# Kernel optimization log

Hardware: AMD Instinct MI355X
Metric: run time of the kernel (lower is better)

## Reference

```python
import jax, jax.numpy as jnp
import numpy as np

CP_LEN = 256
FFT_SIZE = 1024
OFFSET = CP_LEN // 2                      # 128
PILOT_SPACING = 100
NSYMS = 824
TOTAL_SYMS = NSYMS + 1 + NSYMS // PILOT_SPACING   # 833
PAD_L = (FFT_SIZE - TOTAL_SYMS) // 2      # 95
PAD_R = FFT_SIZE - PAD_L - TOTAL_SYMS     # 96
PILOTS_IDX = np.arange(PAD_L, FFT_SIZE - PAD_R, PILOT_SPACING)  # 9 pilots

def _data_indices():
    # Statically unroll the original while-loop: gather all non-pilot data bins.
    idxs = []
    idx = 0
    jj = PAD_L + 1
    while idx < NSYMS:
        n = min(PILOT_SPACING - 1, NSYMS - idx)
        idxs.extend(range(jj, jj + n))
        idx += n
        jj += n + 1
    return np.asarray(idxs, dtype=np.int32)

DATA_IDX = _data_indices()  # [824]


def setup_inputs() -> dict:
    key = jax.random.key(0)
    # [batch, n_symbols, 2*(FFT_SIZE+CP_LEN)] interleaved I/Q floats
    in1 = jax.random.normal(key, (16, 1024, 2 * (FFT_SIZE + CP_LEN)), dtype=jnp.float32)
    return {"in1": in1}


def reference(in1):
    t = jnp.arange(FFT_SIZE, dtype=jnp.float32)
    # Deinterleave I/Q -> complex64
    iq = jax.lax.complex(in1[:, :, ::2], in1[:, :, 1::2])
    # FFT of the window starting at half the CP, then fftshift via roll
    spec = jnp.fft.fft(iq[:, :, OFFSET:OFFSET + FFT_SIZE], axis=2)
    result = jnp.roll(spec, FFT_SIZE // 2, axis=2)
    # Compensate timing-offset phase ramp
    result = result * jnp.exp(1j * OFFSET * t * (2.0 * np.pi / FFT_SIZE))
    # Estimate residual slope from pilot phase differences (wrapped to [-pi,pi])
    a = jnp.diff(jnp.angle(result[:, :, PILOTS_IDX]), axis=2)
    a = jnp.where(a > np.pi, a - 2.0 * np.pi, a)
    a = jnp.where(a < -np.pi, a + 2.0 * np.pi, a)
    mn = jnp.mean(a, axis=2)  # [B, S]
    result = result * jnp.exp(-1j * t * mn[:, :, None] / PILOT_SPACING)
    # Gather data (non-pilot) bins and interleave real/imag -> [B, S, 2*NSYMS]
    data = result[:, :, DATA_IDX]
    x = jnp.stack([data.real, data.imag], axis=-1).reshape(
        data.shape[0], data.shape[1], 2 * NSYMS)
    return x.astype(jnp.float32)
```

## Files before the change

### kernel.cpp

```cpp
#include <hip/hip_runtime.h>
#include <math.h>

#define NT      256
#define NSYMS   824
#define NPILOT  9

#define PADIDX(k) ((k) + ((k) >> 4))

#define C32_TWOPI_1024  6.1359233222901821136474609375e-3f

__device__ __forceinline__ float2 cmulf(float2 a, float2 b) {
    return make_float2(a.x * b.x - a.y * b.y, a.x * b.y + a.y * b.x);
}

template <int LM, int F>
__device__ __forceinline__ void dif_stage(float2* __restrict__ buf,
                                          const float2* __restrict__ W256,
                                          int i) {
    const int r = i & (LM - 1);
    const int base = ((i & ~(LM - 1)) << 2) | r;
    float2 a = buf[PADIDX(base)];
    float2 b = buf[PADIDX(base + LM)];
    float2 c = buf[PADIDX(base + 2 * LM)];
    float2 d = buf[PADIDX(base + 3 * LM)];
    float2 t0 = make_float2(a.x + c.x, a.y + c.y);
    float2 t1 = make_float2(a.x - c.x, a.y - c.y);
    float2 t2 = make_float2(b.x + d.x, b.y + d.y);
    float2 t3 = make_float2(b.x - d.x, b.y - d.y);
    float2 y0 = make_float2(t0.x + t2.x, t0.y + t2.y);
    float2 y1 = make_float2(t1.x + t3.y, t1.y - t3.x);
    float2 y2 = make_float2(t0.x - t2.x, t0.y - t2.y);
    float2 y3 = make_float2(t1.x - t3.y, t1.y + t3.x);
    const int e1 = F * r;
    const int e2 = 2 * F * r;
    const int e3 = 3 * F * r;
    float2 w1 = W256[PADIDX(e1)];
    float2 w2 = W256[PADIDX(e2 & 255)];
    if (e2 & 256) w2 = make_float2(w2.y, -w2.x);
    float2 w3 = W256[PADIDX(e3 & 255)];
    {
        const int q = e3 >> 8;
        if (q == 1)      w3 = make_float2(w3.y, -w3.x);
        else if (q == 2) w3 = make_float2(-w3.x, -w3.y);
    }
    buf[PADIDX(base)]          = y0;
    buf[PADIDX(base + LM)]     = cmulf(w1, y1);
    buf[PADIDX(base + 2 * LM)] = cmulf(w2, y2);
    buf[PADIDX(base + 3 * LM)] = cmulf(w3, y3);
}

__global__ void table_init(double2* __restrict__ Tg, float2* __restrict__ Wg) {
    const int t = threadIdx.x;
    double sn, cs;
    sincos((double)t * -6.1359231515425649189e-3, &sn, &cs);
    Tg[t] = make_double2(cs, sn);
    Wg[t] = make_float2((float)cs, (float)sn);
}

__global__ __launch_bounds__(NT, 8) void ofdm_kernel(const float* __restrict__ in,
                                                     float* __restrict__ out,
                                                     const double2* __restrict__ Tg,
                                                     const float2* __restrict__ Wg) {
    __shared__ double2 T256[256];
    __shared__ double2 u_s[NT];
    __shared__ float2  buf[1088];
    __shared__ float2  W256[272];
    __shared__ double2 pr2[NPILOT];
    __shared__ double  mn_s;

    const int row = blockIdx.x;
    const int tid = threadIdx.x;

    const float2* rin2 = (const float2*)(in + (size_t)row * 2560) + 128;
    float2 v0 = rin2[tid];
    float2 v1 = rin2[tid + 256];
    float2 v2 = rin2[tid + 512];
    float2 v3 = rin2[tid + 768];

    T256[tid] = Tg[tid];
    W256[PADIDX(tid)] = Wg[tid];

    double ux = ((double)v0.x - (double)v2.x) - ((double)v1.y - (double)v3.y);
    double uy = ((double)v0.y - (double)v2.y) + ((double)v1.x - (double)v3.x);

    buf[PADIDX(tid)]       = v0;
    buf[PADIDX(tid + 256)] = v1;
    buf[PADIDX(tid + 512)] = v2;
    buf[PADIDX(tid + 768)] = v3;
    u_s[tid] = make_double2(ux, uy);
    __syncthreads();

    if (tid < 16 * NPILOT) {
        const int p  = tid >> 4;
        const int g  = tid & 15;
        const int jj = 95 + 100 * p;
        const int K  = (jj + 512) & 1023;
        const double sc = (p & 1) ? -0.70710678118654752440
                                  :  0.70710678118654752440;
        int idx = (K * g) & 1023;
        const int step = (K * 16) & 1023;
        double2 acc = make_double2(0.0, 0.0);
        #pragma unroll
        for (int m = 0; m < 8; m++) {
            const int s = g + 16 * m;
            double2 u0 = u_s[s];
            double2 u1 = u_s[s + 128];
            double upx = u0.x + sc * (u1.x - u1.y);
            double upy = u0.y + sc * (u1.x + u1.y);
            double2 w  = T256[idx & 255];
            const int q = idx >> 8;
            double wx = w.x, wy = w.y;
            if (q & 1) { double t = wx; wx = wy; wy = -t; }
            if (q & 2) { wx = -wx; wy = -wy; }
            acc.x += wx * upx - wy * upy;
            acc.y += wx * upy + wy * upx;
            idx = (idx + step) & 1023;
        }
        #pragma unroll
        for (int off = 1; off < 16; off <<= 1) {
            acc.x += __shfl_xor(acc.x, off, 64);
            acc.y += __shfl_xor(acc.y, off, 64);
        }
        if (g == 0) pr2[p] = acc;
    }
    dif_stage<256, 1>(buf, W256, tid);
    __syncthreads();

    dif_stage<64, 4>(buf, W256, tid);
    if (tid >= 192) {
        const int p  = tid - 192;
        const int pc = (p < 8) ? p : 8;
        double2 acc = pr2[pc];
        const int jj = 95 + 100 * pc;
        float th32 = (float)(128 * jj) * C32_TWOPI_1024;
        double sn, cs;
        sincos((double)th32, &sn, &cs);
        double csf = (double)(float)cs;
        double snf = (double)(float)sn;
        double re = acc.x * csf - acc.y * snf;
        double im = acc.x * snf + acc.y * csf;
        double a  = atan2(im, re);
        double an = __shfl_down(a, 1, 64);
        double d  = an - a;
        if (d > 3.14159265358979323846)       d -= 6.28318530717958647693;
        else if (d < -3.14159265358979323846) d += 6.28318530717958647693;
        if (p >= 8) d = 0.0;
        d += __shfl_xor(d, 1, 64);
        d += __shfl_xor(d, 2, 64);
        d += __shfl_xor(d, 4, 64);
        if (p == 0) mn_s = d * 0.125;
    }
    __syncthreads();

    dif_stage<16, 16>(buf, W256, tid);
    __syncthreads();
    dif_stage<4, 64>(buf, W256, tid);
    __syncthreads();

    {
        const double mn001 = mn_s * 0.01;
        const int pb = PADIDX(4 * tid);
        float2 a = buf[pb];
        float2 b = buf[pb + 1];
        float2 c = buf[pb + 2];
        float2 d = buf[pb + 3];
        float2 t0 = make_float2(a.x + c.x, a.y + c.y);
        float2 t1 = make_float2(a.x - c.x, a.y - c.y);
        float2 t2 = make_float2(b.x + d.x, b.y + d.y);
        float2 t3 = make_float2(b.x - d.x, b.y - d.y);
        float2 y0 = make_float2(t0.x + t2.x, t0.y + t2.y);
        float2 y1 = make_float2(t1.x + t3.y, t1.y - t3.x);
        float2 y2 = make_float2(t0.x - t2.x, t0.y - t2.y);
        float2 y3 = make_float2(t1.x - t3.y, t1.y + t3.x);

        const int R = ((tid & 3) << 6) | (((tid >> 2) & 3) << 4) |
                      (((tid >> 4) & 3) << 2) | ((tid >> 6) & 3);

        float2* rout = (float2*)(out + (size_t)row * (2 * NSYMS));
        float2 ys[4] = { y2, y3, y0, y1 };
        #pragma unroll
        for (int k = 0; k < 4; k++) {
            const int jj = R + 256 * k;
            if (jj >= 96 && jj <= 927 && ((jj - 95) % 100) != 0) {
                const int dd = jj - 96 - (jj - 96) / 100;
                float2 z = ys[k];
                float th32 = (float)(128 * jj) * C32_TWOPI_1024;
                float ph = th32 - (float)(mn001 * (double)jj);
                float sn, cs;
                __sincosf(ph, &sn, &cs);
                rout[dd] = make_float2(z.x * cs - z.y * sn,
                                       z.x * sn + z.y * cs);
            }
        }
    }
}

extern "C" void kernel_launch(void* const* d_in, const int* in_sizes, int n_in,
                              void* d_out, int out_size, void* d_ws, size_t ws_size,
                              hipStream_t stream) {
    const float* in = (const float*)d_in[0];
    float* out = (float*)d_out;
    double2* Tg = (double2*)d_ws;
    float2*  Wg = (float2*)((char*)d_ws + 4096);
    table_init<<<dim3(1), dim3(256), 0, stream>>>(Tg, Wg);
    ofdm_kernel<<<dim3(16 * 1024), dim3(NT), 0, stream>>>(in, out, Tg, Wg);
}
```

Before: 267.5 us.

## Do first FFT stage in registers and read twiddles from global memory

```diff
diff --git a/kernel.cpp b/kernel.cpp
--- a/kernel.cpp
+++ b/kernel.cpp
@@ -15,7 +15,7 @@
 
 template <int LM, int F>
 __device__ __forceinline__ void dif_stage(float2* __restrict__ buf,
-                                          const float2* __restrict__ W256,
+                                          const float2* __restrict__ Wg,
                                           int i) {
     const int r = i & (LM - 1);
     const int base = ((i & ~(LM - 1)) << 2) | r;
@@ -34,10 +34,10 @@
     const int e1 = F * r;
     const int e2 = 2 * F * r;
     const int e3 = 3 * F * r;
-    float2 w1 = W256[PADIDX(e1)];
-    float2 w2 = W256[PADIDX(e2 & 255)];
+    float2 w1 = Wg[e1];
+    float2 w2 = Wg[e2 & 255];
     if (e2 & 256) w2 = make_float2(w2.y, -w2.x);
-    float2 w3 = W256[PADIDX(e3 & 255)];
+    float2 w3 = Wg[e3 & 255];
     {
         const int q = e3 >> 8;
         if (q == 1)      w3 = make_float2(w3.y, -w3.x);
@@ -61,10 +61,8 @@
                                                      float* __restrict__ out,
                                                      const double2* __restrict__ Tg,
                                                      const float2* __restrict__ Wg) {
-    __shared__ double2 T256[256];
     __shared__ double2 u_s[NT];
     __shared__ float2  buf[1088];
-    __shared__ float2  W256[272];
     __shared__ double2 pr2[NPILOT];
     __shared__ double  mn_s;
 
@@ -77,16 +75,33 @@
     float2 v2 = rin2[tid + 512];
     float2 v3 = rin2[tid + 768];
 
-    T256[tid] = Tg[tid];
-    W256[PADIDX(tid)] = Wg[tid];
-
     double ux = ((double)v0.x - (double)v2.x) - ((double)v1.y - (double)v3.y);
     double uy = ((double)v0.y - (double)v2.y) + ((double)v1.x - (double)v3.x);
 
-    buf[PADIDX(tid)]       = v0;
-    buf[PADIDX(tid + 256)] = v1;
-    buf[PADIDX(tid + 512)] = v2;
-    buf[PADIDX(tid + 768)] = v3;
+    {
+        const int e2 = 2 * tid, e3 = 3 * tid;
+        float2 w1 = Wg[tid];
+        float2 w2 = Wg[e2 & 255];
+        if (e2 & 256) w2 = make_float2(w2.y, -w2.x);
+        float2 w3 = Wg[e3 & 255];
+        {
+            const int q = e3 >> 8;
+            if (q == 1)      w3 = make_float2(w3.y, -w3.x);
+            else if (q == 2) w3 = make_float2(-w3.x, -w3.y);
+        }
+        float2 t0 = make_float2(v0.x + v2.x, v0.y + v2.y);
+        float2 t1 = make_float2(v0.x - v2.x, v0.y - v2.y);
+        float2 t2 = make_float2(v1.x + v3.x, v1.y + v3.y);
+        float2 t3 = make_float2(v1.x - v3.x, v1.y - v3.y);
+        float2 y0 = make_float2(t0.x + t2.x, t0.y + t2.y);
+        float2 y1 = make_float2(t1.x + t3.y, t1.y - t3.x);
+        float2 y2 = make_float2(t0.x - t2.x, t0.y - t2.y);
+        float2 y3 = make_float2(t1.x - t3.y, t1.y + t3.x);
+        buf[PADIDX(tid)]       = y0;
+        buf[PADIDX(tid + 256)] = cmulf(w1, y1);
+        buf[PADIDX(tid + 512)] = cmulf(w2, y2);
+        buf[PADIDX(tid + 768)] = cmulf(w3, y3);
+    }
     u_s[tid] = make_double2(ux, uy);
     __syncthreads();
 
@@ -107,7 +122,7 @@
             double2 u1 = u_s[s + 128];
             double upx = u0.x + sc * (u1.x - u1.y);
             double upy = u0.y + sc * (u1.x + u1.y);
-            double2 w  = T256[idx & 255];
+            double2 w  = Tg[idx & 255];
             const int q = idx >> 8;
             double wx = w.x, wy = w.y;
             if (q & 1) { double t = wx; wx = wy; wy = -t; }
@@ -123,10 +138,10 @@
         }
         if (g == 0) pr2[p] = acc;
     }
-    dif_stage<256, 1>(buf, W256, tid);
-    __syncthreads();
-
-    dif_stage<64, 4>(buf, W256, tid);
+    dif_stage<64, 4>(buf, Wg, tid);
+    __syncthreads();
+
+    dif_stage<16, 16>(buf, Wg, tid);
     if (tid >= 192) {
         const int p  = tid - 192;
         const int pc = (p < 8) ? p : 8;
@@ -152,9 +167,7 @@
     }
     __syncthreads();
 
-    dif_stage<16, 16>(buf, W256, tid);
-    __syncthreads();
-    dif_stage<4, 64>(buf, W256, tid);
+    dif_stage<4, 64>(buf, Wg, tid);
     __syncthreads();
 
     {
```

Result: slower. 307.4 us (+14.9%).
